# Kernel optimization log

Measured on AMD Instinct MI355X. Metric: run time of the kernel, lower is better.

## Reference

```python
import jax, jax.numpy as jnp
import numpy as np

B, L, D_MODEL = 2, 2048, 1024
D_STATE, D_CONV, EXPAND = 8, 4, 2
D_INNER = EXPAND * D_MODEL          # 2048
DT_RANK = (D_MODEL + 15) // 16      # 64


def setup_inputs() -> dict:
    key = jax.random.key(0)
    ks = jax.random.split(key, 8)
    s = 0.02
    x = jax.random.normal(ks[0], (B, L, D_MODEL), dtype=jnp.float32)
    W_in = jax.random.normal(ks[1], (D_MODEL, 2 * D_INNER), dtype=jnp.float32) * s
    dw_kernel = jax.random.normal(ks[2], (D_CONV, D_INNER), dtype=jnp.float32) * s  # depthwise
    pw_kernel = jax.random.normal(ks[3], (D_INNER, D_INNER), dtype=jnp.float32) * s  # pointwise
    conv_bias = jnp.zeros((D_INNER,), dtype=jnp.float32)
    W_x = jax.random.normal(ks[4], (D_INNER, DT_RANK + 2 * D_STATE), dtype=jnp.float32) * s
    W_dt = jax.random.normal(ks[5], (DT_RANK, D_INNER), dtype=jnp.float32) * s
    b_dt = jnp.zeros((D_INNER,), dtype=jnp.float32)
    # A = repeat(range(1..d_state), d_inner).reshape(d_inner, d_state), stored as log
    A_init = np.repeat(np.arange(1, D_STATE + 1, dtype=np.float32), D_INNER).reshape(D_INNER, D_STATE)
    A_log = jnp.asarray(np.log(A_init))
    D = jnp.ones((D_INNER,), dtype=jnp.float32)
    W_out = jax.random.normal(ks[6], (D_INNER, D_MODEL), dtype=jnp.float32) * s
    return {"x": x, "W_in": W_in, "dw_kernel": dw_kernel, "pw_kernel": pw_kernel,
            "conv_bias": conv_bias, "W_x": W_x, "W_dt": W_dt, "b_dt": b_dt,
            "A_log": A_log, "D": D, "W_out": W_out}


def reference(x, W_in, dw_kernel, pw_kernel, conv_bias, W_x, W_dt, b_dt, A_log, D, W_out):
    d_inner, d_state = A_log.shape
    dt_rank = W_dt.shape[0]
    d_conv = dw_kernel.shape[0]
    bsz = x.shape[0]

    xz = x @ W_in                                   # [B,L,2*di]
    x_in, z = jnp.split(xz, 2, axis=-1)             # each [B,L,di]

    # causal separable conv: depthwise (causal pad) -> pointwise -> swish
    xp = jnp.pad(x_in, ((0, 0), (d_conv - 1, 0), (0, 0)))
    xc = jax.lax.conv_general_dilated(
        xp, dw_kernel[:, None, :], window_strides=(1,), padding='VALID',
        dimension_numbers=('NWC', 'WIO', 'NWC'), feature_group_count=d_inner)
    xc = jax.nn.silu(xc @ pw_kernel + conv_bias)    # [B,L,di]

    x_dbl = xc @ W_x                                # [B,L,dt_rank+2*ds]
    delta = x_dbl[..., :dt_rank]
    Bm = x_dbl[..., dt_rank:dt_rank + d_state]      # [B,L,ds]
    C = x_dbl[..., dt_rank + d_state:]              # [B,L,ds]
    delta = jax.nn.softplus(delta @ W_dt + b_dt)    # [B,L,di]

    A = -jnp.exp(A_log)                             # [di,ds]
    deltaA = jnp.exp(jnp.einsum('bld,dn->bldn', delta, A))       # [B,L,di,ds]
    deltaB_u = jnp.einsum('bld,bln,bld->bldn', delta, Bm, xc)    # [B,L,di,ds]

    def step(h, inp):
        dA_t, dBu_t, C_t = inp
        h = dA_t * h + dBu_t                        # [B,di,ds]
        y_t = jnp.einsum('bn,bdn->bd', C_t, h)      # [B,di]
        return h, y_t

    h0 = jnp.zeros((bsz, d_inner, d_state), dtype=x.dtype)
    elems = (deltaA.transpose(1, 0, 2, 3), deltaB_u.transpose(1, 0, 2, 3), C.transpose(1, 0, 2))
    _, ys = jax.lax.scan(step, h0, elems)           # ys: [L,B,di]
    y = ys.transpose(1, 0, 2)                       # [B,L,di]

    y = y + xc * D
    y = y * jax.nn.silu(z)
    return y @ W_out                                # [B,L,d_model]
```

## Files before the change

kernel.cpp:

```cpp
#include <hip/hip_runtime.h>
#include <math.h>

#define Bb 2
#define Ll 2048
#define DMODEL 1024
#define DINNER 2048
#define DSTATE 8
#define DTRANK 64
#define DCONV 4
#define MM (Bb*Ll)
#define NCH 64
#define CL 32
#define G3_KCH 8
#define G3_KC (DINNER / G3_KCH)

typedef __attribute__((ext_vector_type(8))) short    bf16x8;
typedef __attribute__((ext_vector_type(4))) float    f32x4;

__device__ __forceinline__ float silu_f(float x) {
    return x / (1.0f + __expf(-x));
}
__device__ __forceinline__ float softplus_f(float x) {
    return fmaxf(x, 0.0f) + log1pf(__expf(-fabsf(x)));
}
__device__ __forceinline__ unsigned short f2bf(float f) {
    unsigned int u = __float_as_uint(f);
    u += 0x7fffu + ((u >> 16) & 1u);
    return (unsigned short)(u >> 16);
}
__device__ __forceinline__ float bf2f(unsigned short u) {
    return __uint_as_float(((unsigned int)u) << 16);
}
__device__ __forceinline__ void async_cp16(const unsigned short* g, unsigned short* l) {
    __builtin_amdgcn_global_load_lds(
        (const __attribute__((address_space(1))) void*)g,
        (__attribute__((address_space(3))) void*)l, 16, 0, 0);
}

template <int EPI, int NW, int TN, typename OT, int RX = 0, int RY = 1>
__global__ __launch_bounds__(NW * 64, 4) void mfma_gemm(
    const unsigned short* __restrict__ A, const unsigned short* __restrict__ Bt,
    OT* __restrict__ C, OT* __restrict__ C2, int nsplit,
    int M, int N, int K, int lda, int ldb, int ldc,
    const float* __restrict__ bias)
{
    constexpr int NT   = NW * 64;
    constexpr int WNC  = NW / 2;
    constexpr int WNE  = TN / WNC;
    constexpr int NJ   = WNE / 16;
    constexpr int RPP  = NT / 4;
    constexpr int APASS = 128 / RPP;
    constexpr int BPASS = TN / RPP;

    __shared__ unsigned short As[2][128 * 32];
    __shared__ unsigned short Bs[2][TN * 32];

    int bxx = blockIdx.x, byy = blockIdx.y;
    if constexpr (RX > 0) {
        const int f = blockIdx.y * gridDim.x + blockIdx.x;
        const int c = f & 7, q = f >> 3;
        const int rgw = gridDim.x / RX;
        bxx = (c % rgw) * RX + (q % RX);
        byy = (c / rgw) * RY + (q / RX);
    }
    const int bm = byy * 128;
    const int bn = bxx * TN;
    const int tid  = threadIdx.x;
    const int w    = tid >> 6;
    const int lane = tid & 63;
    const int wm = (w / WNC) * 64;
    const int wn = (w % WNC) * WNE;
    const int lr = lane & 15;
    const int lq = lane >> 4;

    const int row  = tid >> 2;
    const int sp   = tid & 3;
    const int slog = sp ^ ((row >> 1) & 3);
    const unsigned short* gA = A  + (size_t)(bm + row) * lda + slog * 8;
    const unsigned short* gB = Bt + (size_t)(bn + row) * ldb + slog * 8;
    const int st = tid * 8;

    const int fsw = (lq ^ ((lr >> 1) & 3)) * 8;

    f32x4 acc[4][NJ];
#pragma unroll
    for (int i = 0; i < 4; ++i)
#pragma unroll
        for (int j = 0; j < NJ; ++j) acc[i][j] = (f32x4){0.f, 0.f, 0.f, 0.f};

#pragma unroll
    for (int p = 0; p < APASS; ++p)
        async_cp16(gA + (size_t)p * RPP * lda, &As[0][p * RPP * 32 + st]);
#pragma unroll
    for (int p = 0; p < BPASS; ++p)
        async_cp16(gB + (size_t)p * RPP * ldb, &Bs[0][p * RPP * 32 + st]);

    int cur = 0;
    for (int k0 = 0; k0 < K; k0 += 32, cur ^= 1) {
        __syncthreads();
        const int nk = k0 + 32;
        if (nk < K) {
            const int nb = cur ^ 1;
#pragma unroll
            for (int p = 0; p < APASS; ++p)
                async_cp16(gA + (size_t)p * RPP * lda + nk, &As[nb][p * RPP * 32 + st]);
#pragma unroll
            for (int p = 0; p < BPASS; ++p)
                async_cp16(gB + (size_t)p * RPP * ldb + nk, &Bs[nb][p * RPP * 32 + st]);
        }

        bf16x8 a[4], b[NJ];
#pragma unroll
        for (int i = 0; i < 4; ++i)
            a[i] = *(const bf16x8*)&As[cur][(wm + i * 16 + lr) * 32 + fsw];
#pragma unroll
        for (int j = 0; j < NJ; ++j)
            b[j] = *(const bf16x8*)&Bs[cur][(wn + j * 16 + lr) * 32 + fsw];
#pragma unroll
        for (int i = 0; i < 4; ++i)
#pragma unroll
            for (int j = 0; j < NJ; ++j)
                acc[i][j] = __builtin_amdgcn_mfma_f32_16x16x32_bf16(
                    a[i], b[j], acc[i][j], 0, 0, 0);
    }

#pragma unroll
    for (int i = 0; i < 4; ++i) {
        const int row0 = bm + wm + i * 16 + lq * 4;
#pragma unroll
        for (int j = 0; j < NJ; ++j) {
            const int col = bn + wn + j * 16 + lr;
            OT* Cb; int colb;
            if (col < nsplit) { Cb = C; colb = col; }
            else              { Cb = C2; colb = col - nsplit; }
            float bv = (EPI != 0) ? bias[col] : 0.0f;
#pragma unroll
            for (int r = 0; r < 4; ++r) {
                float v = acc[i][j][r];
                if (EPI == 1) v = silu_f(v + bv);
                if (EPI == 2) v = softplus_f(v + bv);
                if (sizeof(OT) == 2)
                    Cb[(size_t)(row0 + r) * ldc + colb] = (OT)f2bf(v);
                else
                    Cb[(size_t)(row0 + r) * ldc + colb] = (OT)v;
            }
        }
    }
}

template <bool I1, bool I2, int VMA, int VMB>
__device__ __forceinline__ void g1_tile(
    int kt, const unsigned short* __restrict__ gA,
    const unsigned short* __restrict__ gB, int lda, int ldb,
    unsigned short* As, unsigned short* Bs, int st,
    int wm, int wn, int lr, int fsw, f32x4 (&acc)[8][4])
{
    const int cur = kt & 1;
    const int sb0 = (cur << 1) * 8192;
    const int sb1 = ((cur << 1) | 1) * 8192;
    const int nb1 = ((kt + 1) & 1) << 1;
    const int nb2 = ((kt + 2) & 1) << 1;
    bf16x8 a[4], b[4];

#pragma unroll
    for (int i = 0; i < 4; ++i)
        a[i] = *(const bf16x8*)&As[sb0 + (wm + i * 16 + lr) * 32 + fsw];
#pragma unroll
    for (int j = 0; j < 4; ++j)
        b[j] = *(const bf16x8*)&Bs[sb0 + (wn + j * 16 + lr) * 32 + fsw];
    if (I1) {
        const unsigned short* s = gA + (kt + 1) * 64 + 32;
        unsigned short* d = &As[(nb1 | 1) * 8192 + st];
        async_cp16(s, d);
        async_cp16(s + (size_t)128 * lda, d + 4096);
        __builtin_amdgcn_sched_barrier(0);
    }
    __builtin_amdgcn_s_barrier();
    asm volatile("s_waitcnt lgkmcnt(0)" ::: "memory");
    __builtin_amdgcn_sched_barrier(0);
    __builtin_amdgcn_s_setprio(1);
#pragma unroll
    for (int i = 0; i < 4; ++i)
#pragma unroll
        for (int j = 0; j < 4; ++j)
            acc[i][j] = __builtin_amdgcn_mfma_f32_16x16x32_bf16(
                a[i], b[j], acc[i][j], 0, 0, 0);
    __builtin_amdgcn_s_setprio(0);
    __builtin_amdgcn_s_barrier();

#pragma unroll
    for (int i = 0; i < 4; ++i)
        a[i] = *(const bf16x8*)&As[sb0 + (wm + (4 + i) * 16 + lr) * 32 + fsw];
    if (I1) {
        const unsigned short* s = gB + (kt + 1) * 64 + 32;
        unsigned short* d = &Bs[(nb1 | 1) * 8192 + st];
        async_cp16(s, d);
        async_cp16(s + (size_t)128 * ldb, d + 4096);
        __builtin_amdgcn_sched_barrier(0);
    }
    __builtin_amdgcn_s_barrier();
    asm volatile("s_waitcnt lgkmcnt(0)" ::: "memory");
    __builtin_amdgcn_sched_barrier(0);
    __builtin_amdgcn_s_setprio(1);
#pragma unroll
    for (int i = 0; i < 4; ++i)
#pragma unroll
        for (int j = 0; j < 4; ++j)
            acc[4 + i][j] = __builtin_amdgcn_mfma_f32_16x16x32_bf16(
                a[i], b[j], acc[4 + i][j], 0, 0, 0);
    __builtin_amdgcn_s_setprio(0);
    asm volatile("s_waitcnt vmcnt(%0)" :: "n"(VMA) : "memory");
    __builtin_amdgcn_s_barrier();

#pragma unroll
    for (int i = 0; i < 4; ++i)
        a[i] = *(const bf16x8*)&As[sb1 + (wm + i * 16 + lr) * 32 + fsw];
#pragma unroll
    for (int j = 0; j < 4; ++j)
        b[j] = *(const bf16x8*)&Bs[sb1 + (wn + j * 16 + lr) * 32 + fsw];
    if (I2) {
        const unsigned short* s = gA + (kt + 2) * 64;
        unsigned short* d = &As[nb2 * 8192 + st];
        async_cp16(s, d);
        async_cp16(s + (size_t)128 * lda, d + 4096);
        __builtin_amdgcn_sched_barrier(0);
    }
    __builtin_amdgcn_s_barrier();
    asm volatile("s_waitcnt lgkmcnt(0)" ::: "memory");
    __builtin_amdgcn_sched_barrier(0);
    __builtin_amdgcn_s_setprio(1);
#pragma unroll
    for (int i = 0; i < 4; ++i)
#pragma unroll
        for (int j = 0; j < 4; ++j)
            acc[i][j] = __builtin_amdgcn_mfma_f32_16x16x32_bf16(
                a[i], b[j], acc[i][j], 0, 0, 0);
    __builtin_amdgcn_s_setprio(0);
    __builtin_amdgcn_s_barrier();

#pragma unroll
    for (int i = 0; i < 4; ++i)
        a[i] = *(const bf16x8*)&As[sb1 + (wm + (4 + i) * 16 + lr) * 32 + fsw];
    if (I2) {
        const unsigned short* s = gB + (kt + 2) * 64;
        unsigned short* d = &Bs[nb2 * 8192 + st];
        async_cp16(s, d);
        async_cp16(s + (size_t)128 * ldb, d + 4096);
        __builtin_amdgcn_sched_barrier(0);
    }
    __builtin_amdgcn_s_barrier();
    asm volatile("s_waitcnt lgkmcnt(0)" ::: "memory");
    __builtin_amdgcn_sched_barrier(0);
    __builtin_amdgcn_s_setprio(1);
#pragma unroll
    for (int i = 0; i < 4; ++i)
#pragma unroll
        for (int j = 0; j < 4; ++j)
            acc[4 + i][j] = __builtin_amdgcn_mfma_f32_16x16x32_bf16(
                a[i], b[j], acc[4 + i][j], 0, 0, 0);
    __builtin_amdgcn_s_setprio(0);
    asm volatile("s_waitcnt vmcnt(%0)" :: "n"(VMB) : "memory");
    __builtin_amdgcn_s_barrier();
}

__global__ __launch_bounds__(512, 2) void gemm256_g1(
    const unsigned short* __restrict__ A, const unsigned short* __restrict__ Bt,
    unsigned short* __restrict__ Cx, unsigned short* __restrict__ Cz,
    int K, int lda, int ldb, int ldc, int nsplit)
{
    __shared__ unsigned short As[4 * 8192];
    __shared__ unsigned short Bs[4 * 8192];

    int bx, by;
    {
        const int f = blockIdx.y * gridDim.x + blockIdx.x;
        const int c = f & 7, q = f >> 3;
        const int rgw = gridDim.x >> 3;
        bx = (c % rgw) * 8 + (q & 7);
        by = (c / rgw) * 4 + (q >> 3);
    }
    const int bm = by * 256, bn = bx * 256;
    const int tid  = threadIdx.x;
    const int lane = tid & 63;
    const int w    = tid >> 6;
    const int wm = (w >> 2) << 7;
    const int wn = (w & 3) << 6;
    const int lr = lane & 15;
    const int lq = lane >> 4;
    const int fsw = (lq ^ ((lr >> 1) & 3)) * 8;

    const int row  = tid >> 2;
    const int slog = (tid & 3) ^ ((row >> 1) & 3);
    const unsigned short* gA = A  + (size_t)(bm + row) * lda + slog * 8;
    const unsigned short* gB = Bt + (size_t)(bn + row) * ldb + slog * 8;
    const int st = tid * 8;
    const int NT = K >> 6;

    f32x4 acc[8][4];
#pragma unroll
    for (int i = 0; i < 8; ++i)
#pragma unroll
        for (int j = 0; j < 4; ++j) acc[i][j] = (f32x4){0.f, 0.f, 0.f, 0.f};

    auto stg = [&](const unsigned short* g, int ld, unsigned short* d) {
        async_cp16(g, d);
        async_cp16(g + (size_t)128 * ld, d + 4096);
    };
    stg(gA,      lda, As + 0 * 8192 + st);
    __builtin_amdgcn_sched_barrier(0);
    stg(gB,      ldb, Bs + 0 * 8192 + st);
    __builtin_amdgcn_sched_barrier(0);
    stg(gA + 32, lda, As + 1 * 8192 + st);
    __builtin_amdgcn_sched_barrier(0);
    stg(gB + 32, ldb, Bs + 1 * 8192 + st);
    __builtin_amdgcn_sched_barrier(0);
    stg(gA + 64, lda, As + 2 * 8192 + st);
    __builtin_amdgcn_sched_barrier(0);
    stg(gB + 64, ldb, Bs + 2 * 8192 + st);
    asm volatile("s_waitcnt vmcnt(8)" ::: "memory");
    __builtin_amdgcn_sched_barrier(0);
    __builtin_amdgcn_s_barrier();

    for (int kt = 0; kt + 2 < NT; ++kt)
        g1_tile<true, true, 8, 8>(kt, gA, gB, lda, ldb,
                                  As, Bs, st, wm, wn, lr, fsw, acc);
    g1_tile<true,  false, 8, 4>(NT - 2, gA, gB, lda, ldb,
                                As, Bs, st, wm, wn, lr, fsw, acc);
    g1_tile<false, false, 0, 0>(NT - 1, gA, gB, lda, ldb,
                                As, Bs, st, wm, wn, lr, fsw, acc);

#pragma unroll
    for (int i = 0; i < 8; ++i) {
        const int row0 = bm + wm + i * 16 + lq * 4;
#pragma unroll
        for (int j = 0; j < 4; ++j) {
            const int col = bn + wn + j * 16 + lr;
            unsigned short* Cb; int colb;
            if (col < nsplit) { Cb = Cx; colb = col; }
            else              { Cb = Cz; colb = col - nsplit; }
#pragma unroll
            for (int r = 0; r < 4; ++r)
                Cb[(size_t)(row0 + r) * ldc + colb] = f2bf(acc[i][j][r]);
        }
    }
}

__global__ __launch_bounds__(256) void prep_all(
    const float* __restrict__ x, const float* __restrict__ W_in,
    const float* __restrict__ pwk, const float* __restrict__ W_out,
    const float* __restrict__ W_dt,
    unsigned short* __restrict__ x_bf, unsigned short* __restrict__ Wint,
    unsigned short* __restrict__ pw_t, unsigned short* __restrict__ Woutt,
    unsigned short* __restrict__ Wdtt)
{
    const int b = blockIdx.x;
    const int t = threadIdx.x;
    if (b < 4096) {
        int i = b * 1024 + t * 4;
        float4 v = *(const float4*)&x[i];
        ushort4 o;
        o.x = f2bf(v.x); o.y = f2bf(v.y); o.z = f2bf(v.z); o.w = f2bf(v.w);
        *(ushort4*)&x_bf[i] = o;
        return;
    }
    const float* src; unsigned short* dst; int R, C, c0, r0;
    if (b < 8192) {
        int bi = b - 4096; src = W_in; dst = Wint; R = 1024; C = 4096;
        c0 = (bi & 127) * 32; r0 = (bi >> 7) * 32;
    } else if (b < 12288) {
        int bi = b - 8192; src = pwk; dst = pw_t; R = 2048; C = 2048;
        c0 = (bi & 63) * 32; r0 = (bi >> 6) * 32;
    } else if (b < 14336) {
        int bi = b - 12288; src = W_out; dst = Woutt; R = 2048; C = 1024;
        c0 = (bi & 31) * 32; r0 = (bi >> 5) * 32;
    } else {
        int bi = b - 14336; src = W_dt; dst = Wdtt; R = 64; C = 2048;
        c0 = (bi & 63) * 32; r0 = (bi >> 6) * 32;
    }
    __shared__ float tile[32][33];
    const int tx = t & 31;
    const int ty = t >> 5;
#pragma unroll
    for (int i = 0; i < 32; i += 8)
        tile[ty + i][tx] = src[(size_t)(r0 + ty + i) * C + c0 + tx];
    __syncthreads();
#pragma unroll
    for (int i = 0; i < 32; i += 8)
        dst[(size_t)(c0 + ty + i) * R + r0 + tx] = f2bf(tile[tx][ty + i]);
}

__global__ __launch_bounds__(256) void g3_splitk(
    const unsigned short* __restrict__ xc, const float* __restrict__ Wx,
    float* __restrict__ part)
{
    __shared__ float As[16][68];
    __shared__ float Bs[16][85];
    const int m0 = blockIdx.x * 64;
    const int kb = blockIdx.y * G3_KC;
    const int t = threadIdx.x;
    const int tr = t >> 4;
    const int tc = t & 15;

    const int arow = t >> 2;
    const int ak4  = (t & 3) * 4;
    const int bk   = t >> 4;
    const int bc   = (t & 15) * 5;

    float acc[4][5];
#pragma unroll
    for (int r = 0; r < 4; ++r)
#pragma unroll
        for (int c = 0; c < 5; ++c) acc[r][c] = 0.0f;

    for (int k0 = 0; k0 < G3_KC; k0 += 16) {
        ushort4 av = *(const ushort4*)&xc[(size_t)(m0 + arow) * DINNER + kb + k0 + ak4];
        float bv[5];
#pragma unroll
        for (int q = 0; q < 5; ++q)
            bv[q] = Wx[(size_t)(kb + k0 + bk) * 80 + bc + q];
        __syncthreads();
        As[ak4 + 0][arow] = bf2f(av.x);
        As[ak4 + 1][arow] = bf2f(av.y);
        As[ak4 + 2][arow] = bf2f(av.z);
        As[ak4 + 3][arow] = bf2f(av.w);
#pragma unroll
        for (int q = 0; q < 5; ++q) Bs[bk][bc + q] = bv[q];
        __syncthreads();
#pragma unroll
        for (int k = 0; k < 16; ++k) {
            float a[4], b[5];
#pragma unroll
            for (int r = 0; r < 4; ++r) a[r] = As[k][tr * 4 + r];
#pragma unroll
            for (int c = 0; c < 5; ++c) b[c] = Bs[k][tc * 5 + c];
#pragma unroll
            for (int r = 0; r < 4; ++r)
#pragma unroll
                for (int c = 0; c < 5; ++c)
                    acc[r][c] = fmaf(a[r], b[c], acc[r][c]);
        }
    }
#pragma unroll
    for (int r = 0; r < 4; ++r)
#pragma unroll
        for (int c = 0; c < 5; ++c)
            part[((size_t)blockIdx.y * MM + m0 + tr * 4 + r) * 80 + tc * 5 + c] = acc[r][c];
}

__global__ __launch_bounds__(256) void g3_reduce(
    const float* __restrict__ part, float* __restrict__ xdbl,
    unsigned short* __restrict__ xdbl64)
{
    int i = (blockIdx.x * 256 + threadIdx.x) * 4;
    if (i >= MM * 80) return;
    float4 s = *(const float4*)&part[i];
#pragma unroll
    for (int c = 1; c < G3_KCH; ++c) {
        float4 p = *(const float4*)&part[(size_t)c * MM * 80 + i];
        s.x += p.x; s.y += p.y; s.z += p.z; s.w += p.w;
    }
    *(float4*)&xdbl[i] = s;
    int col = i % 80;
    if (col < 64) {
        int row = i / 80;
        ushort4 o;
        o.x = f2bf(s.x); o.y = f2bf(s.y); o.z = f2bf(s.z); o.w = f2bf(s.w);
        *(ushort4*)&xdbl64[(size_t)row * 64 + col] = o;
    }
}

__global__ __launch_bounds__(256) void dwconv_kernel(
    const unsigned short* __restrict__ x_in, const float* __restrict__ dwk,
    unsigned short* __restrict__ out)
{
    int i4 = blockIdx.x * 256 + threadIdx.x;
    if (i4 >= MM * DINNER / 4) return;
    int d = (i4 * 4) & (DINNER - 1);
    int bl = (i4 * 4) >> 11;
    int l = bl & (Ll - 1);
    int b = bl >> 11;
    float a0 = 0.f, a1 = 0.f, a2 = 0.f, a3 = 0.f;
#pragma unroll
    for (int k = 0; k < DCONV; ++k) {
        int t = l + k - (DCONV - 1);
        if (t >= 0) {
            ushort4 xv = *(const ushort4*)&x_in[(size_t)(b * Ll + t) * DINNER + d];
            float4 wv = *(const float4*)&dwk[k * DINNER + d];
            a0 = fmaf(bf2f(xv.x), wv.x, a0);
            a1 = fmaf(bf2f(xv.y), wv.y, a1);
            a2 = fmaf(bf2f(xv.z), wv.z, a2);
            a3 = fmaf(bf2f(xv.w), wv.w, a3);
        }
    }
    ushort4 o;
    o.x = f2bf(a0); o.y = f2bf(a1); o.z = f2bf(a2); o.w = f2bf(a3);
    *(ushort4*)&out[i4 * 4] = o;
}

__global__ __launch_bounds__(256) void scan_pass1(
    const float* __restrict__ delta, const unsigned short* __restrict__ xc,
    const float* __restrict__ xdbl, const float* __restrict__ A_log,
    float* __restrict__ cs_a, float* __restrict__ cs_h)
{
    const int d = blockIdx.x * 256 + threadIdx.x;
    const int c = blockIdx.y;
    const int b = blockIdx.z;
    const int t0 = c * CL;

    __shared__ float sB[CL][8];
    {
        int i = threadIdx.x;
        int t = i >> 3, j = i & 7;
        sB[t][j] = xdbl[((size_t)(b * Ll + t0 + t)) * 80 + DTRANK + j];
    }
    __syncthreads();

    float An[8];
#pragma unroll
    for (int n = 0; n < 8; ++n) An[n] = -__expf(A_log[d * 8 + n]);

    float h[8], ap[8];
#pragma unroll
    for (int n = 0; n < 8; ++n) { h[n] = 0.0f; ap[n] = 1.0f; }

    const float* dptr = delta + ((size_t)(b * Ll + t0)) * DINNER + d;
    const unsigned short* xptr = xc + ((size_t)(b * Ll + t0)) * DINNER + d;

#pragma unroll 4
    for (int t = 0; t < CL; ++t) {
        float dl = dptr[(size_t)t * DINNER];
        float xv = bf2f(xptr[(size_t)t * DINNER]);
        float du = dl * xv;
#pragma unroll
        for (int n = 0; n < 8; ++n) {
            float dA = __expf(dl * An[n]);
            h[n] = fmaf(dA, h[n], du * sB[t][n]);
            ap[n] *= dA;
        }
    }

    size_t base = (((size_t)(b * NCH + c)) * 8) * DINNER + d;
#pragma unroll
    for (int n = 0; n < 8; ++n) {
        cs_a[base + (size_t)n * DINNER] = ap[n];
        cs_h[base + (size_t)n * DINNER] = h[n];
    }
}

__global__ __launch_bounds__(256) void scan_pass2(
    const float* __restrict__ cs_a, const float* cs_h, float* hin)
{
    int idx = blockIdx.x * 256 + threadIdx.x;
    if (idx >= Bb * 8 * DINNER) return;
    int d = idx & (DINNER - 1);
    int n = (idx >> 11) & 7;
    int b = idx >> 14;
    float H = 0.0f;
#pragma unroll 4
    for (int c = 0; c < NCH; ++c) {
        size_t o = (((size_t)(b * NCH + c)) * 8 + n) * DINNER + d;
        float a = cs_a[o];
        float hh = cs_h[o];
        hin[o] = H;
        H = fmaf(a, H, hh);
    }
}

__global__ __launch_bounds__(256) void scan_pass3(
    const float* __restrict__ delta, const unsigned short* __restrict__ xc,
    const float* __restrict__ xdbl, const float* __restrict__ A_log,
    const float* __restrict__ hin, const unsigned short* __restrict__ z,
    const float* __restrict__ Dvec, unsigned short* __restrict__ y_bf)
{
    const int d = blockIdx.x * 256 + threadIdx.x;
    const int c = blockIdx.y;
    const int b = blockIdx.z;
    const int t0 = c * CL;

    __shared__ float sB[CL][8];
    __shared__ float sC[CL][8];
    {
        int i = threadIdx.x;
        int t = i >> 4, j = i & 15;
        float v = xdbl[((size_t)(b * Ll + t0 + t)) * 80 + DTRANK + j];
        if (j < 8) sB[t][j] = v; else sC[t][j - 8] = v;
        t = (i + 256) >> 4; j = (i + 256) & 15;
        v = xdbl[((size_t)(b * Ll + t0 + t)) * 80 + DTRANK + j];
        if (j < 8) sB[t][j] = v; else sC[t][j - 8] = v;
    }
    __syncthreads();

    float An[8];
#pragma unroll
    for (int n = 0; n < 8; ++n) An[n] = -__expf(A_log[d * 8 + n]);

    float h[8];
    size_t hbase = (((size_t)(b * NCH + c)) * 8) * DINNER + d;
#pragma unroll
    for (int n = 0; n < 8; ++n) h[n] = hin[hbase + (size_t)n * DINNER];

    const float Dd = Dvec[d];
    const float* dptr = delta + ((size_t)(b * Ll + t0)) * DINNER + d;
    const unsigned short* xptr = xc + ((size_t)(b * Ll + t0)) * DINNER + d;
    const unsigned short* zptr = z + ((size_t)(b * Ll + t0)) * DINNER + d;
    unsigned short* yptr = y_bf + ((size_t)(b * Ll + t0)) * DINNER + d;

    for (int t = 0; t < CL; ++t) {
        float dl = dptr[(size_t)t * DINNER];
        float xv = bf2f(xptr[(size_t)t * DINNER]);
        float du = dl * xv;
        float yt = 0.0f;
#pragma unroll
        for (int n = 0; n < 8; ++n) {
            float dA = __expf(dl * An[n]);
            h[n] = fmaf(dA, h[n], du * sB[t][n]);
            yt = fmaf(sC[t][n], h[n], yt);
        }
        float zv = bf2f(zptr[(size_t)t * DINNER]);
        yptr[(size_t)t * DINNER] = f2bf((yt + xv * Dd) * silu_f(zv));
    }
}

extern "C" void kernel_launch(void* const* d_in, const int* in_sizes, int n_in,
                              void* d_out, int out_size, void* d_ws, size_t ws_size,
                              hipStream_t stream)
{
    const float* x         = (const float*)d_in[0];
    const float* W_in      = (const float*)d_in[1];
    const float* dwk       = (const float*)d_in[2];
    const float* pwk       = (const float*)d_in[3];
    const float* conv_bias = (const float*)d_in[4];
    const float* W_x       = (const float*)d_in[5];
    const float* W_dt      = (const float*)d_in[6];
    const float* b_dt      = (const float*)d_in[7];
    const float* A_log     = (const float*)d_in[8];
    const float* Dv        = (const float*)d_in[9];
    const float* W_out     = (const float*)d_in[10];
    float* out = (float*)d_out;

    char* ws = (char*)d_ws;
    unsigned short* x_in_bf = (unsigned short*)(ws);
    unsigned short* z_bf    = (unsigned short*)(ws + (16ull << 20));
    float*          delta   = (float*)(ws + (32ull << 20));
    unsigned short* x_bf    = (unsigned short*)(ws + (64ull << 20));
    unsigned short* y_bf    = (unsigned short*)(ws + (64ull << 20));
    unsigned short* Wint    = (unsigned short*)(ws + (72ull << 20));
    unsigned short* pw_t    = (unsigned short*)(ws + (80ull << 20));
    unsigned short* xcp_bf  = (unsigned short*)(ws + (88ull << 20));
    unsigned short* xc_bf   = (unsigned short*)(ws + (104ull << 20));
    unsigned short* Woutt   = (unsigned short*)(ws + (120ull << 20));
    float*          xdbl    = (float*)(ws + (124ull << 20));
    unsigned short* xdbl64  = (unsigned short*)(ws + (125ull << 20) + (512ull << 10));
    float*          g3part  = (float*)(ws + (126ull << 20));
    float*          cs_a    = (float*)(ws + (136ull << 20));
    float*          cs_h    = (float*)(ws + (144ull << 20));
    unsigned short* Wdtt    = (unsigned short*)(ws + (152ull << 20));
    float*          hin     = cs_h;
    dim3 blk(256);

    prep_all<<<14464, blk, 0, stream>>>(x, W_in, pwk, W_out, W_dt,
                                        x_bf, Wint, pw_t, Woutt, Wdtt);

    gemm256_g1<<<dim3((2 * DINNER) / 256, MM / 256), dim3(512), 0, stream>>>(
        x_bf, Wint, x_in_bf, z_bf,
        DMODEL, DMODEL, DMODEL, DINNER,
        DINNER);

    dwconv_kernel<<<MM * DINNER / 4 / 256, blk, 0, stream>>>(x_in_bf, dwk, xcp_bf);

    mfma_gemm<1, 8, 128, unsigned short, 8, 8>
        <<<dim3(DINNER / 128, MM / 128), dim3(512), 0, stream>>>(
        xcp_bf, pw_t, xc_bf, xc_bf, DINNER + 1,
        MM, DINNER, DINNER, DINNER, DINNER, DINNER, conv_bias);

    g3_splitk<<<dim3(MM / 64, G3_KCH), blk, 0, stream>>>(xc_bf, W_x, g3part);
    g3_reduce<<<(MM * 80 / 4 + 255) / 256, blk, 0, stream>>>(g3part, xdbl, xdbl64);

    mfma_gemm<2, 4, 128, float, 8, 8>
        <<<dim3(DINNER / 128, MM / 128), blk, 0, stream>>>(
        xdbl64, Wdtt, delta, delta, DINNER + 1,
        MM, DINNER, DTRANK, DTRANK, DTRANK, DINNER, b_dt);

    scan_pass1<<<dim3(DINNER / 256, NCH, Bb), blk, 0, stream>>>(
        delta, xc_bf, xdbl, A_log, cs_a, cs_h);
    scan_pass2<<<(Bb * 8 * DINNER + 255) / 256, blk, 0, stream>>>(cs_a, cs_h, hin);
    scan_pass3<<<dim3(DINNER / 256, NCH, Bb), blk, 0, stream>>>(
        delta, xc_bf, xdbl, A_log, hin, z_bf, Dv, y_bf);

    mfma_gemm<0, 4, 64, float, 8, 8>
        <<<dim3(DMODEL / 64, MM / 128), blk, 0, stream>>>(
        y_bf, Woutt, out, out, DMODEL + 1,
        MM, DMODEL, DINNER, DINNER, DINNER, DMODEL, nullptr);
}
```

Before: 369.8 us.

## Use 256x128 double-buffered async-copy GEMM for pointwise conv

```diff
diff --git a/kernel.cpp b/kernel.cpp
--- a/kernel.cpp
+++ b/kernel.cpp
@@ -341,6 +341,164 @@
 #pragma unroll
             for (int r = 0; r < 4; ++r)
                 Cb[(size_t)(row0 + r) * ldc + colb] = f2bf(acc[i][j][r]);
+        }
+    }
+}
+
+template <bool I1, bool I2, int VMA, int VMB>
+__device__ __forceinline__ void g2_tile(
+    int kt, const unsigned short* __restrict__ gA,
+    const unsigned short* __restrict__ gB, int lda, int ldb,
+    unsigned short* As, unsigned short* Bs, int st,
+    int wm, int wn, int lr, int fsw, f32x4 (&acc)[4][4])
+{
+    const int cur = kt & 1;
+    const int sa0 = (cur << 1) * 8192;
+    const int sa1 = ((cur << 1) | 1) * 8192;
+    const int sb0 = (cur << 1) * 4096;
+    const int sb1 = ((cur << 1) | 1) * 4096;
+    const int nb1 = (((kt + 1) & 1) << 1) | 1;
+    const int nb2 = ((kt + 2) & 1) << 1;
+    bf16x8 a[4], b[4];
+
+#pragma unroll
+    for (int i = 0; i < 4; ++i)
+        a[i] = *(const bf16x8*)&As[sa0 + (wm + i * 16 + lr) * 32 + fsw];
+#pragma unroll
+    for (int j = 0; j < 4; ++j)
+        b[j] = *(const bf16x8*)&Bs[sb0 + (wn + j * 16 + lr) * 32 + fsw];
+    if (I1) {
+        const unsigned short* sA = gA + (kt + 1) * 64 + 32;
+        unsigned short* dA = &As[nb1 * 8192 + st];
+        async_cp16(sA, dA);
+        async_cp16(sA + (size_t)128 * lda, dA + 4096);
+        async_cp16(gB + (kt + 1) * 64 + 32, &Bs[nb1 * 4096 + st]);
+        __builtin_amdgcn_sched_barrier(0);
+    }
+    __builtin_amdgcn_s_barrier();
+    asm volatile("s_waitcnt lgkmcnt(0)" ::: "memory");
+    __builtin_amdgcn_sched_barrier(0);
+    __builtin_amdgcn_s_setprio(1);
+#pragma unroll
+    for (int i = 0; i < 4; ++i)
+#pragma unroll
+        for (int j = 0; j < 4; ++j)
+            acc[i][j] = __builtin_amdgcn_mfma_f32_16x16x32_bf16(
+                a[i], b[j], acc[i][j], 0, 0, 0);
+    __builtin_amdgcn_s_setprio(0);
+    asm volatile("s_waitcnt vmcnt(%0)" :: "n"(VMA) : "memory");
+    __builtin_amdgcn_s_barrier();
+
+#pragma unroll
+    for (int i = 0; i < 4; ++i)
+        a[i] = *(const bf16x8*)&As[sa1 + (wm + i * 16 + lr) * 32 + fsw];
+#pragma unroll
+    for (int j = 0; j < 4; ++j)
+        b[j] = *(const bf16x8*)&Bs[sb1 + (wn + j * 16 + lr) * 32 + fsw];
+    if (I2) {
+        const unsigned short* sA = gA + (kt + 2) * 64;
+        unsigned short* dA = &As[nb2 * 8192 + st];
+        async_cp16(sA, dA);
+        async_cp16(sA + (size_t)128 * lda, dA + 4096);
+        async_cp16(gB + (kt + 2) * 64, &Bs[nb2 * 4096 + st]);
+        __builtin_amdgcn_sched_barrier(0);
+    }
+    __builtin_amdgcn_s_barrier();
+    asm volatile("s_waitcnt lgkmcnt(0)" ::: "memory");
+    __builtin_amdgcn_sched_barrier(0);
+    __builtin_amdgcn_s_setprio(1);
+#pragma unroll
+    for (int i = 0; i < 4; ++i)
+#pragma unroll
+        for (int j = 0; j < 4; ++j)
+            acc[i][j] = __builtin_amdgcn_mfma_f32_16x16x32_bf16(
+                a[i], b[j], acc[i][j], 0, 0, 0);
+    __builtin_amdgcn_s_setprio(0);
+    asm volatile("s_waitcnt vmcnt(%0)" :: "n"(VMB) : "memory");
+    __builtin_amdgcn_s_barrier();
+}
+
+template <int EPI, typename OT>
+__global__ __launch_bounds__(512, 2) void gemm256x128(
+    const unsigned short* __restrict__ A, const unsigned short* __restrict__ Bt,
+    OT* __restrict__ C, int K, int lda, int ldb, int ldc,
+    const float* __restrict__ bias)
+{
+    __shared__ unsigned short As[4 * 8192];
+    __shared__ unsigned short Bs[4 * 4096];
+
+    int bx, by;
+    {
+        const int f = blockIdx.y * gridDim.x + blockIdx.x;
+        const int c = f & 7, q = f >> 3;
+        const int rgw = gridDim.x >> 3;
+        bx = (c % rgw) * 8 + (q & 7);
+        by = (c / rgw) * 4 + (q >> 3);
+    }
+    const int bm = by * 256, bn = bx * 128;
+    const int tid  = threadIdx.x;
+    const int lane = tid & 63;
+    const int w    = tid >> 6;
+    const int wm = (w >> 1) << 6;
+    const int wn = (w & 1) << 6;
+    const int lr = lane & 15;
+    const int lq = lane >> 4;
+    const int fsw = (lq ^ ((lr >> 1) & 3)) * 8;
+
+    const int row  = tid >> 2;
+    const int slog = (tid & 3) ^ ((row >> 1) & 3);
+    const unsigned short* gA = A  + (size_t)(bm + row) * lda + slog * 8;
+    const unsigned short* gB = Bt + (size_t)(bn + row) * ldb + slog * 8;
+    const int st = tid * 8;
+    const int NT = K >> 6;
+
+    f32x4 acc[4][4];
+#pragma unroll
+    for (int i = 0; i < 4; ++i)
+#pragma unroll
+        for (int j = 0; j < 4; ++j) acc[i][j] = (f32x4){0.f, 0.f, 0.f, 0.f};
+
+    auto stg = [&](int ko, int slot) {
+        const unsigned short* sA = gA + ko;
+        unsigned short* dA = &As[slot * 8192 + st];
+        async_cp16(sA, dA);
+        async_cp16(sA + (size_t)128 * lda, dA + 4096);
+        async_cp16(gB + ko, &Bs[slot * 4096 + st]);
+    };
+    stg(0, 0);
+    __builtin_amdgcn_sched_barrier(0);
+    stg(32, 1);
+    __builtin_amdgcn_sched_barrier(0);
+    stg(64, 2);
+    asm volatile("s_waitcnt vmcnt(6)" ::: "memory");
+    __builtin_amdgcn_sched_barrier(0);
+    __builtin_amdgcn_s_barrier();
+
+    for (int kt = 0; kt + 2 < NT; ++kt)
+        g2_tile<true, true, 6, 6>(kt, gA, gB, lda, ldb,
+                                  As, Bs, st, wm, wn, lr, fsw, acc);
+    g2_tile<true,  false, 6, 3>(NT - 2, gA, gB, lda, ldb,
+                                As, Bs, st, wm, wn, lr, fsw, acc);
+    g2_tile<false, false, 0, 0>(NT - 1, gA, gB, lda, ldb,
+                                As, Bs, st, wm, wn, lr, fsw, acc);
+
+#pragma unroll
+    for (int i = 0; i < 4; ++i) {
+        const int row0 = bm + wm + i * 16 + lq * 4;
+#pragma unroll
+        for (int j = 0; j < 4; ++j) {
+            const int col = bn + wn + j * 16 + lr;
+            float bv = (EPI != 0) ? bias[col] : 0.0f;
+#pragma unroll
+            for (int r = 0; r < 4; ++r) {
+                float v = acc[i][j][r];
+                if (EPI == 1) v = silu_f(v + bv);
+                if (EPI == 2) v = softplus_f(v + bv);
+                if (sizeof(OT) == 2)
+                    C[(size_t)(row0 + r) * ldc + col] = (OT)f2bf(v);
+                else
+                    C[(size_t)(row0 + r) * ldc + col] = (OT)v;
+            }
         }
     }
 }
@@ -668,10 +826,10 @@
 
     dwconv_kernel<<<MM * DINNER / 4 / 256, blk, 0, stream>>>(x_in_bf, dwk, xcp_bf);
 
-    mfma_gemm<1, 8, 128, unsigned short, 8, 8>
-        <<<dim3(DINNER / 128, MM / 128), dim3(512), 0, stream>>>(
-        xcp_bf, pw_t, xc_bf, xc_bf, DINNER + 1,
-        MM, DINNER, DINNER, DINNER, DINNER, DINNER, conv_bias);
+    gemm256x128<1, unsigned short>
+        <<<dim3(DINNER / 128, MM / 256), dim3(512), 0, stream>>>(
+        xcp_bf, pw_t, xc_bf,
+        DINNER, DINNER, DINNER, DINNER, conv_bias);
 
     g3_splitk<<<dim3(MM / 64, G3_KCH), blk, 0, stream>>>(xc_bf, W_x, g3part);
     g3_reduce<<<(MM * 80 / 4 + 255) / 256, blk, 0, stream>>>(g3part, xdbl, xdbl64);
```

New measurement: 362.8 us. No clear change (-1.9%).
